# Kernel tuning notes

Measured on AMD Instinct MI355X. Metric: run time of the kernel, lower is better.

The kernel has to match this reference:

```python
import jax, jax.numpy as jnp
import numpy as np

B, T, S, H, E, V = 32, 64, 64, 512, 512, 32000

def setup_inputs() -> dict:
    key = jax.random.key(0)
    ks = jax.random.split(key, 16)
    sd = 0.02
    return {
        "inputs": jax.random.randint(ks[0], (B, T), 0, V),
        "encoder_outputs": jax.random.normal(ks[1], (B, S, 2 * H), jnp.float32),
        "h0": jax.random.normal(ks[2], (B, H), jnp.float32),
        "c0": jax.random.normal(ks[3], (B, H), jnp.float32),
        "emb": jax.random.normal(ks[4], (V, E), jnp.float32) * sd,
        "W_ih": jax.random.normal(ks[5], (4 * H, E), jnp.float32) * sd,
        "W_hh": jax.random.normal(ks[6], (4 * H, H), jnp.float32) * sd,
        "b_ih": jnp.zeros((4 * H,), jnp.float32),
        "b_hh": jnp.zeros((4 * H,), jnp.float32),
        "W_att": jax.random.normal(ks[7], (2 * H, H), jnp.float32) * sd,
        "W_comb": jax.random.normal(ks[8], (H, 3 * H), jnp.float32) * sd,
        "b_comb": jnp.zeros((H,), jnp.float32),
        "W_out": jax.random.normal(ks[9], (V, H), jnp.float32) * sd,
        "b_out": jnp.zeros((V,), jnp.float32),
    }

def reference(inputs, encoder_outputs, h0, c0, emb, W_ih, W_hh, b_ih, b_hh,
              W_att, W_comb, b_comb, W_out, b_out):
    x = emb[inputs]                      # [B,T,E]
    xs = jnp.swapaxes(x, 0, 1)           # [T,B,E] for scan

    def step(carry, x_t):
        h, c = carry
        # torch LSTM gate order: i, f, g, o
        gates = x_t @ W_ih.T + h @ W_hh.T + b_ih + b_hh   # [B,4H]
        i, f, g, o = jnp.split(gates, 4, axis=-1)
        c = jax.nn.sigmoid(f) * c + jax.nn.sigmoid(i) * jnp.tanh(g)
        h = jax.nn.sigmoid(o) * jnp.tanh(c)
        # attention (note: no softmax in original module)
        q = h @ W_att.T                                     # [B,2H]
        w = jnp.einsum('bd,bsd->bs', q, encoder_outputs)    # [B,S]
        applied = jnp.einsum('bs,bsd->bd', w, encoder_outputs)  # [B,2H]
        merged = jnp.concatenate([h, applied], axis=-1)     # [B,3H]
        out = jnp.tanh(merged @ W_comb.T + b_comb)          # [B,H]
        return (h, c), out

    (h, c), outs = jax.lax.scan(step, (h0, c0), xs)
    outs = jnp.swapaxes(outs, 0, 1)      # [B,T,H]
    logits = outs @ W_out.T + b_out      # [B,T,V]
    return logits, h, c
```

## Files before the change

### kernel.cpp

```cpp
#include <hip/hip_runtime.h>
#include <hip/hip_fp16.h>

typedef _Float16 f16;
typedef _Float16 f16x4 __attribute__((ext_vector_type(4)));
typedef _Float16 f16x8 __attribute__((ext_vector_type(8)));
typedef float    f32x4 __attribute__((ext_vector_type(4)));

#define DEV __device__ __forceinline__

constexpr int B = 32, T = 64, S = 64, H = 512, E = 512, V = 32000;
constexpr int BT = B * T;
constexpr int G4 = 4 * H;
constexpr int NBLK = 64;

DEV float sigf(float x) { return 1.f / (1.f + expf(-x)); }

DEV unsigned long long ld_u64_cg(const unsigned long long* p) {
    return __hip_atomic_load(p, __ATOMIC_RELAXED, __HIP_MEMORY_SCOPE_AGENT);
}
DEV unsigned int ld_u32_cg(const unsigned int* p) {
    return __hip_atomic_load(p, __ATOMIC_RELAXED, __HIP_MEMORY_SCOPE_AGENT);
}
DEV void st_u32_cg(unsigned int* p, unsigned int v) {
    __hip_atomic_store(p, v, __ATOMIC_RELAXED, __HIP_MEMORY_SCOPE_AGENT);
}


__global__ __launch_bounds__(256) void cvt_f16(const float* __restrict__ s,
                                               f16* __restrict__ d, int n4) {
    for (int i = blockIdx.x * blockDim.x + threadIdx.x; i < n4;
         i += gridDim.x * blockDim.x) {
        float4 v = ((const float4*)s)[i];
        f16x4 o = {(f16)v.x, (f16)v.y, (f16)v.z, (f16)v.w};
        ((f16x4*)d)[i] = o;
    }
}

__global__ __launch_bounds__(256) void pack_wfrag(const float* __restrict__ W,
                                                  f16* __restrict__ Wf) {
    int id = blockIdx.x * 256 + threadIdx.x;
    if (id >= NBLK * 2 * 16 * 64) return;
    int lane = id & 63;
    int ks = (id >> 6) & 15;
    int ni = (id >> 10) & 1;
    int n = id >> 11;
    int cl = ni * 16 + (lane & 15);
    int ul = cl >> 2, g = cl & 3;
    int unit = n * 8 + ul;
    int k = ks * 32 + (lane >> 4) * 8;
    const float* src = W + (size_t)(g * 512 + unit) * 512 + k;
    float4 a = *(const float4*)src;
    float4 b = *(const float4*)(src + 4);
    f16x8 o = {(f16)a.x, (f16)a.y, (f16)a.z, (f16)a.w,
               (f16)b.x, (f16)b.y, (f16)b.z, (f16)b.w};
    *(f16x8*)(Wf + (size_t)id * 8) = o;
}

__global__ __launch_bounds__(256) void gather_x(const int* __restrict__ tok,
                                                const float* __restrict__ emb,
                                                f16* __restrict__ x) {
    int id = blockIdx.x * blockDim.x + threadIdx.x;
    if (id >= BT * (E / 4)) return;
    int row = id >> 7;
    int e4 = (id & 127) * 4;
    int t = tok[row];
    float4 v = *(const float4*)(emb + (size_t)t * E + e4);
    f16x4 o = {(f16)v.x, (f16)v.y, (f16)v.z, (f16)v.w};
    ((f16x4*)x)[id] = o;
}

__global__ __launch_bounds__(256) void init_h0(const float* __restrict__ h0,
                                               f16* __restrict__ xbuf,
                                               unsigned int* __restrict__ fl) {
    int i = blockIdx.x * 256 + threadIdx.x;
    if (i < B * H) {
        int nn = i >> 8;
        int bb = (i >> 3) & 31;
        int ul = i & 7;
        xbuf[i] = (f16)h0[bb * 512 + nn * 8 + ul];
    }
    if (i < NBLK) fl[i] = 0u;
}


template <bool BIAS, bool B2, bool TANH, bool PERM, bool MSWAP, typename OUT>
__global__ __launch_bounds__(256) void gemm_bt(
    const f16* __restrict__ A, int lda, const f16* __restrict__ W, int ldw,
    OUT* __restrict__ C, int ldc, int K, const float* __restrict__ bias1,
    const float* __restrict__ bias2) {
    __shared__ f16 smA[128 * 32];
    __shared__ f16 smB[128 * 32];
    const int tid = threadIdx.x;
    const int lane = tid & 63;
    const int wv = tid >> 6;
    const int wr = wv >> 1, wc = wv & 1;
    const int m0 = (MSWAP ? blockIdx.x : blockIdx.y) * 128;
    const int n0 = (MSWAP ? blockIdx.y : blockIdx.x) * 128;

    const int ar0 = tid >> 2;
    const int kq = (tid & 3) * 8;

    f32x4 acc[4][4];
#pragma unroll
    for (int m = 0; m < 4; m++)
#pragma unroll
        for (int n = 0; n < 4; n++) acc[m][n] = {0.f, 0.f, 0.f, 0.f};

    const int arow = wr * 64 + (lane & 15);
    const int brow = wc * 64 + (lane & 15);
    const int kk = (lane >> 4) * 8;

    const int ksteps = K >> 5;
    for (int s = 0; s < ksteps; ++s) {
        const int k0 = s * 32;
        const f16* Ag = A + (size_t)(m0 + ar0) * lda + k0 + kq;
        const f16* Wg = W + (size_t)(n0 + ar0) * ldw + k0 + kq;
        uint4 va0 = *(const uint4*)Ag;
        uint4 va1 = *(const uint4*)(Ag + (size_t)64 * lda);
        uint4 vb0 = *(const uint4*)Wg;
        uint4 vb1 = *(const uint4*)(Wg + (size_t)64 * ldw);
        __syncthreads();
        *(uint4*)(smA + tid * 8) = va0;
        *(uint4*)(smA + (tid + 256) * 8) = va1;
        *(uint4*)(smB + tid * 8) = vb0;
        *(uint4*)(smB + (tid + 256) * 8) = vb1;
        __syncthreads();
        f16x8 af[4], bfr[4];
#pragma unroll
        for (int m = 0; m < 4; m++)
            af[m] = *(const f16x8*)(smA + (arow + m * 16) * 32 + kk);
#pragma unroll
        for (int n = 0; n < 4; n++)
            bfr[n] = *(const f16x8*)(smB + (brow + n * 16) * 32 + kk);
#pragma unroll
        for (int m = 0; m < 4; m++)
#pragma unroll
            for (int n = 0; n < 4; n++)
                acc[m][n] = __builtin_amdgcn_mfma_f32_16x16x32_f16(
                    af[m], bfr[n], acc[m][n], 0, 0, 0);
    }

    const int fr = lane & 15, fq = lane >> 4;
#pragma unroll
    for (int m = 0; m < 4; m++) {
        const int row0 = m0 + wr * 64 + m * 16 + fq * 4;
#pragma unroll
        for (int n = 0; n < 4; n++) {
            const int col = n0 + wc * 64 + n * 16 + fr;
            float bb = 0.f;
            if (BIAS) bb += bias1[col];
            if (B2) bb += bias2[col];
            int nb = 0, cl = 0;
            if (PERM) {
                int g = col >> 9;
                int unit = col & 511;
                nb = unit >> 3;
                cl = ((unit & 7) << 2) | g;
            }
#pragma unroll
            for (int r = 0; r < 4; r++) {
                float v = acc[m][n][r] + bb;
                if (TANH) v = tanhf(v);
                if (PERM) {
                    int bt = row0 + r;
                    int b_ = bt >> 6, tt = bt & 63;
                    C[((size_t)(tt * 64 + nb) * 32 + b_) * 32 + cl] = (OUT)v;
                } else {
                    C[(size_t)(row0 + r) * ldc + col] = (OUT)v;
                }
            }
        }
    }
}


__global__ __launch_bounds__(256, 1) void lstm_scan6(
    const float* __restrict__ gxp, const f16* __restrict__ Wfrag,
    const float* __restrict__ c0, f16* __restrict__ xbuf,
    unsigned int* __restrict__ flags, f16* __restrict__ merged,
    float* __restrict__ hout, float* __restrict__ cout) {
    const int n = blockIdx.x;
    const int tid = threadIdx.x;
    const int lane = tid & 63, wv = tid >> 6;
    const int mi = wv >> 1, ni = wv & 1;
    __shared__ f16 hst[32][520];
    __shared__ float gl[32][32];

    f16x8 bf[16];
    const f16* wbase = Wfrag + (size_t)((n * 2 + ni) * 16) * 512 + lane * 8;
#pragma unroll
    for (int ks = 0; ks < 16; ks++) bf[ks] = *(const f16x8*)(wbase + ks * 512);

    const int bb = tid >> 3, ul = tid & 7;
    const int unit = n * 8 + ul;
    float c = c0[bb * 512 + unit];
    float h = 0.f;

    const int sb = (tid & 63) >> 1;
    const int su0 = (tid & 1) * 4;

    const int arow = mi * 16 + (lane & 15);
    const int kcol0 = (lane >> 4) * 8;
    const int fr = lane & 15, fq = lane >> 4;

    for (int t = 0; t < T; ++t) {
        float4 gx4 = *(const float4*)(gxp +
                                      ((size_t)(t * NBLK + n) * 32 + bb) * 32 +
                                      ul * 4);
        for (;;) {
            unsigned int v = ld_u32_cg(flags + lane);
            if (__all(v >= (unsigned int)t)) break;
            __builtin_amdgcn_s_sleep(1);
        }
        asm volatile("" ::: "memory");
        const unsigned long long* src =
            (const unsigned long long*)(xbuf + (t & 1) * (B * H));
        unsigned long long v[16];
#pragma unroll
        for (int i = 0; i < 16; i++) v[i] = ld_u64_cg(src + i * 256 + tid);
#pragma unroll
        for (int i = 0; i < 16; i++) {
            int np = i * 4 + wv;
            *(unsigned long long*)(&hst[sb][np * 8 + su0]) = v[i];
        }
        __syncthreads();
        f32x4 acc0 = {0.f, 0.f, 0.f, 0.f}, acc1 = {0.f, 0.f, 0.f, 0.f};
#pragma unroll
        for (int ks = 0; ks < 16; ks++) {
            f16x8 af = *(const f16x8*)(&hst[arow][ks * 32 + kcol0]);
            if (ks & 1)
                acc1 = __builtin_amdgcn_mfma_f32_16x16x32_f16(af, bf[ks], acc1,
                                                              0, 0, 0);
            else
                acc0 = __builtin_amdgcn_mfma_f32_16x16x32_f16(af, bf[ks], acc0,
                                                              0, 0, 0);
        }
#pragma unroll
        for (int r = 0; r < 4; r++)
            gl[mi * 16 + fq * 4 + r][ni * 16 + fr] = acc0[r] + acc1[r];
        __syncthreads();
        float4 gv = *(const float4*)&gl[bb][ul * 4];
        float gi = gv.x + gx4.x;
        float gf = gv.y + gx4.y;
        float gg = gv.z + gx4.z;
        float go = gv.w + gx4.w;
        c = sigf(gf) * c + sigf(gi) * tanhf(gg);
        h = sigf(go) * tanhf(c);
        f16 hh = (f16)h;
        unsigned hv = (unsigned)__builtin_bit_cast(unsigned short, hh);
        unsigned other = (unsigned)__shfl_xor((int)hv, 1);
        f16* xn = xbuf + ((t + 1) & 1) * (B * H);
        if ((ul & 1) == 0) {
            st_u32_cg((unsigned int*)(xn + n * 256 + bb * 8 + ul),
                      hv | (other << 16));
        }
        if (t < T - 1) {
            asm volatile("s_waitcnt vmcnt(0)" ::: "memory");
            __syncthreads();
            if (tid == 0) st_u32_cg(flags + n, (unsigned int)(t + 1));
        } else {
            __syncthreads();
        }
        merged[(size_t)(bb * 64 + t) * 1536 + unit] = hh;
    }
    hout[bb * 512 + unit] = h;
    cout[bb * 512 + unit] = c;
}


__global__ __launch_bounds__(256) void attn_apply(const float* __restrict__ q,
                                                  const float* __restrict__ enc,
                                                  f16* __restrict__ merged) {
    const int bt = blockIdx.x;
    const int b = bt >> 6;
    const int tid = threadIdx.x;
    __shared__ float qs[1024];
    __shared__ float ws[64];

    const float* qrow = q + (size_t)bt * 1024;
    *(float4*)(qs + tid * 4) = *(const float4*)(qrow + tid * 4);
    __syncthreads();

    const int wv = tid >> 6, lane = tid & 63;
    const float* encb = enc + (size_t)b * S * 1024;
    for (int s = wv * 16; s < wv * 16 + 16; ++s) {
        const float* er = encb + (size_t)s * 1024;
        float p = 0.f;
#pragma unroll
        for (int i = 0; i < 16; ++i) p += qs[lane + 64 * i] * er[lane + 64 * i];
#pragma unroll
        for (int off = 32; off; off >>= 1) p += __shfl_xor(p, off);
        if (lane == 0) ws[s] = p;
    }
    __syncthreads();

    float a0 = 0.f, a1 = 0.f, a2 = 0.f, a3 = 0.f;
    for (int s = 0; s < 64; ++s) {
        float w = ws[s];
        const float* er = encb + (size_t)s * 1024;
        a0 += w * er[tid];
        a1 += w * er[tid + 256];
        a2 += w * er[tid + 512];
        a3 += w * er[tid + 768];
    }
    f16* mrow = merged + (size_t)bt * 1536 + 512;
    mrow[tid] = (f16)a0;
    mrow[tid + 256] = (f16)a1;
    mrow[tid + 512] = (f16)a2;
    mrow[tid + 768] = (f16)a3;
}


extern "C" void kernel_launch(void* const* d_in, const int* in_sizes, int n_in,
                              void* d_out, int out_size, void* d_ws,
                              size_t ws_size, hipStream_t stream) {
    const int* tok = (const int*)d_in[0];
    const float* enc = (const float*)d_in[1];
    const float* h0 = (const float*)d_in[2];
    const float* c0 = (const float*)d_in[3];
    const float* emb = (const float*)d_in[4];
    const float* W_ih = (const float*)d_in[5];
    const float* W_hh = (const float*)d_in[6];
    const float* b_ih = (const float*)d_in[7];
    const float* b_hh = (const float*)d_in[8];
    const float* W_att = (const float*)d_in[9];
    const float* W_comb = (const float*)d_in[10];
    const float* b_comb = (const float*)d_in[11];
    const float* W_out = (const float*)d_in[12];
    const float* b_out = (const float*)d_in[13];

    float* out_logits = (float*)d_out;
    float* out_h = out_logits + (size_t)BT * V;
    float* out_c = out_h + (size_t)B * H;

    char* p = (char*)d_ws;
    auto alloc = [&](size_t bytes) -> void* {
        void* r = (void*)p;
        p += (bytes + 255) & ~(size_t)255;
        return r;
    };
    f16* W_ih_h = (f16*)alloc((size_t)G4 * E * 2);
    f16* Wfrag = (f16*)alloc((size_t)NBLK * 2 * 16 * 64 * 8 * 2);
    f16* W_att_h = (f16*)alloc((size_t)1024 * 512 * 2);
    f16* W_comb_h = (f16*)alloc((size_t)512 * 1536 * 2);
    f16* W_out_h = (f16*)alloc((size_t)V * 512 * 2);
    f16* x_h = (f16*)alloc((size_t)BT * E * 2);
    float* gxp = (float*)alloc((size_t)T * NBLK * 32 * 32 * 4);
    f16* merged = (f16*)alloc((size_t)BT * 1536 * 2);
    float* qbuf = (float*)alloc((size_t)BT * 1024 * 4);
    f16* outs_h = (f16*)alloc((size_t)BT * 512 * 2);
    f16* xbuf = (f16*)alloc((size_t)2 * B * H * 2);
    unsigned int* flags = (unsigned int*)alloc(256);

    cvt_f16<<<512, 256, 0, stream>>>(W_ih, W_ih_h, G4 * E / 4);
    cvt_f16<<<512, 256, 0, stream>>>(W_att, W_att_h, 1024 * 512 / 4);
    cvt_f16<<<512, 256, 0, stream>>>(W_comb, W_comb_h, 512 * 1536 / 4);
    cvt_f16<<<2048, 256, 0, stream>>>(W_out, W_out_h, V * 512 / 4);
    pack_wfrag<<<512, 256, 0, stream>>>(W_hh, Wfrag);
    gather_x<<<1024, 256, 0, stream>>>(tok, emb, x_h);
    init_h0<<<64, 256, 0, stream>>>(h0, xbuf, flags);

    gemm_bt<true, true, false, true, false, float>
        <<<dim3(16, 16), 256, 0, stream>>>(x_h, E, W_ih_h, E, gxp, 0, E, b_ih,
                                           b_hh);

    lstm_scan6<<<NBLK, 256, 0, stream>>>(gxp, Wfrag, c0, xbuf, flags, merged,
                                         out_h, out_c);

    gemm_bt<false, false, false, false, false, float>
        <<<dim3(8, 16), 256, 0, stream>>>(merged, 1536, W_att_h, 512, qbuf,
                                          1024, 512, nullptr, nullptr);

    attn_apply<<<BT, 256, 0, stream>>>(qbuf, enc, merged);

    gemm_bt<true, false, true, false, false, f16>
        <<<dim3(4, 16), 256, 0, stream>>>(merged, 1536, W_comb_h, 1536, outs_h,
                                          512, 1536, b_comb, nullptr);

    gemm_bt<true, false, false, false, true, float>
        <<<dim3(16, 250), 256, 0, stream>>>(outs_h, 512, W_out_h, 512,
                                            out_logits, V, 512, b_out,
                                            nullptr);
}
```

Baseline: 557.3 us.

## Read h directly in MFMA layout, stage scan outputs, fuse W_out conversion into GEMM

Result: slower. 608.8 us (+9.2%).

```diff
diff --git a/kernel.cpp b/kernel.cpp
--- a/kernel.cpp
+++ b/kernel.cpp
@@ -82,12 +82,24 @@
     if (i < NBLK) fl[i] = 0u;
 }
 
-
-template <bool BIAS, bool B2, bool TANH, bool PERM, bool MSWAP, typename OUT>
+__global__ __launch_bounds__(256) void scatter_h(const f16* __restrict__ mtmp,
+                                                 f16* __restrict__ merged) {
+    int c = blockIdx.x * 256 + threadIdx.x;
+    if (c >= T * NBLK * B) return;
+    int bb = c & 31;
+    int n = (c >> 5) & 63;
+    int t = c >> 11;
+    uint4 v = ((const uint4*)mtmp)[c];
+    ((uint4*)merged)[(size_t)(bb * 64 + t) * 192 + n] = v;
+}
+
+
+template <bool BIAS, bool B2, bool TANH, bool PERM, bool MSWAP, bool WF32,
+          typename OUT>
 __global__ __launch_bounds__(256) void gemm_bt(
-    const f16* __restrict__ A, int lda, const f16* __restrict__ W, int ldw,
-    OUT* __restrict__ C, int ldc, int K, const float* __restrict__ bias1,
-    const float* __restrict__ bias2) {
+    const f16* __restrict__ A, int lda, const f16* __restrict__ W,
+    const float* __restrict__ W32, int ldw, OUT* __restrict__ C, int ldc,
+    int K, const float* __restrict__ bias1, const float* __restrict__ bias2) {
     __shared__ f16 smA[128 * 32];
     __shared__ f16 smB[128 * 32];
     const int tid = threadIdx.x;
@@ -114,11 +126,26 @@
     for (int s = 0; s < ksteps; ++s) {
         const int k0 = s * 32;
         const f16* Ag = A + (size_t)(m0 + ar0) * lda + k0 + kq;
-        const f16* Wg = W + (size_t)(n0 + ar0) * ldw + k0 + kq;
         uint4 va0 = *(const uint4*)Ag;
         uint4 va1 = *(const uint4*)(Ag + (size_t)64 * lda);
-        uint4 vb0 = *(const uint4*)Wg;
-        uint4 vb1 = *(const uint4*)(Wg + (size_t)64 * ldw);
+        uint4 vb0, vb1;
+        if (WF32) {
+            const float* Wg = W32 + (size_t)(n0 + ar0) * ldw + k0 + kq;
+            float4 b00 = *(const float4*)Wg;
+            float4 b01 = *(const float4*)(Wg + 4);
+            float4 b10 = *(const float4*)(Wg + (size_t)64 * ldw);
+            float4 b11 = *(const float4*)(Wg + (size_t)64 * ldw + 4);
+            f16x8 h0v = {(f16)b00.x, (f16)b00.y, (f16)b00.z, (f16)b00.w,
+                         (f16)b01.x, (f16)b01.y, (f16)b01.z, (f16)b01.w};
+            f16x8 h1v = {(f16)b10.x, (f16)b10.y, (f16)b10.z, (f16)b10.w,
+                         (f16)b11.x, (f16)b11.y, (f16)b11.z, (f16)b11.w};
+            vb0 = __builtin_bit_cast(uint4, h0v);
+            vb1 = __builtin_bit_cast(uint4, h1v);
+        } else {
+            const f16* Wg = W + (size_t)(n0 + ar0) * ldw + k0 + kq;
+            vb0 = *(const uint4*)Wg;
+            vb1 = *(const uint4*)(Wg + (size_t)64 * ldw);
+        }
         __syncthreads();
         *(uint4*)(smA + tid * 8) = va0;
         *(uint4*)(smA + (tid + 256) * 8) = va1;
@@ -174,16 +201,15 @@
 }
 
 
-__global__ __launch_bounds__(256, 1) void lstm_scan6(
+__global__ __launch_bounds__(256, 1) void lstm_scan7(
     const float* __restrict__ gxp, const f16* __restrict__ Wfrag,
     const float* __restrict__ c0, f16* __restrict__ xbuf,
-    unsigned int* __restrict__ flags, f16* __restrict__ merged,
+    unsigned int* __restrict__ flags, f16* __restrict__ mtmp,
     float* __restrict__ hout, float* __restrict__ cout) {
     const int n = blockIdx.x;
     const int tid = threadIdx.x;
     const int lane = tid & 63, wv = tid >> 6;
     const int mi = wv >> 1, ni = wv & 1;
-    __shared__ f16 hst[32][520];
     __shared__ float gl[32][32];
 
     f16x8 bf[16];
@@ -196,12 +222,9 @@
     float c = c0[bb * 512 + unit];
     float h = 0.f;
 
-    const int sb = (tid & 63) >> 1;
-    const int su0 = (tid & 1) * 4;
-
-    const int arow = mi * 16 + (lane & 15);
-    const int kcol0 = (lane >> 4) * 8;
     const int fr = lane & 15, fq = lane >> 4;
+    const int arow = mi * 16 + fr;
+    const int ubase = fq * 64 + arow * 2;
 
     for (int t = 0; t < T; ++t) {
         float4 gx4 = *(const float4*)(gxp +
@@ -213,21 +236,20 @@
             __builtin_amdgcn_s_sleep(1);
         }
         asm volatile("" ::: "memory");
-        const unsigned long long* src =
+        const unsigned long long* xb =
             (const unsigned long long*)(xbuf + (t & 1) * (B * H));
-        unsigned long long v[16];
-#pragma unroll
-        for (int i = 0; i < 16; i++) v[i] = ld_u64_cg(src + i * 256 + tid);
-#pragma unroll
-        for (int i = 0; i < 16; i++) {
-            int np = i * 4 + wv;
-            *(unsigned long long*)(&hst[sb][np * 8 + su0]) = v[i];
-        }
-        __syncthreads();
+        unsigned long long lo[16], hi[16];
+#pragma unroll
+        for (int ks = 0; ks < 16; ks++) {
+            lo[ks] = ld_u64_cg(xb + ks * 256 + ubase);
+            hi[ks] = ld_u64_cg(xb + ks * 256 + ubase + 1);
+        }
         f32x4 acc0 = {0.f, 0.f, 0.f, 0.f}, acc1 = {0.f, 0.f, 0.f, 0.f};
 #pragma unroll
         for (int ks = 0; ks < 16; ks++) {
-            f16x8 af = *(const f16x8*)(&hst[arow][ks * 32 + kcol0]);
+            f16x4 l4 = __builtin_bit_cast(f16x4, lo[ks]);
+            f16x4 h4 = __builtin_bit_cast(f16x4, hi[ks]);
+            f16x8 af = {l4.x, l4.y, l4.z, l4.w, h4.x, h4.y, h4.z, h4.w};
             if (ks & 1)
                 acc1 = __builtin_amdgcn_mfma_f32_16x16x32_f16(af, bf[ks], acc1,
                                                               0, 0, 0);
@@ -258,10 +280,8 @@
             asm volatile("s_waitcnt vmcnt(0)" ::: "memory");
             __syncthreads();
             if (tid == 0) st_u32_cg(flags + n, (unsigned int)(t + 1));
-        } else {
-            __syncthreads();
-        }
-        merged[(size_t)(bb * 64 + t) * 1536 + unit] = hh;
+        }
+        mtmp[(size_t)(t * NBLK + n) * 256 + tid] = hh;
     }
     hout[bb * 512 + unit] = h;
     cout[bb * 512 + unit] = c;
@@ -343,42 +363,44 @@
     f16* Wfrag = (f16*)alloc((size_t)NBLK * 2 * 16 * 64 * 8 * 2);
     f16* W_att_h = (f16*)alloc((size_t)1024 * 512 * 2);
     f16* W_comb_h = (f16*)alloc((size_t)512 * 1536 * 2);
-    f16* W_out_h = (f16*)alloc((size_t)V * 512 * 2);
     f16* x_h = (f16*)alloc((size_t)BT * E * 2);
     float* gxp = (float*)alloc((size_t)T * NBLK * 32 * 32 * 4);
     f16* merged = (f16*)alloc((size_t)BT * 1536 * 2);
     float* qbuf = (float*)alloc((size_t)BT * 1024 * 4);
     f16* outs_h = (f16*)alloc((size_t)BT * 512 * 2);
     f16* xbuf = (f16*)alloc((size_t)2 * B * H * 2);
+    f16* mtmp = (f16*)alloc((size_t)T * NBLK * 256 * 2);
     unsigned int* flags = (unsigned int*)alloc(256);
 
     cvt_f16<<<512, 256, 0, stream>>>(W_ih, W_ih_h, G4 * E / 4);
     cvt_f16<<<512, 256, 0, stream>>>(W_att, W_att_h, 1024 * 512 / 4);
     cvt_f16<<<512, 256, 0, stream>>>(W_comb, W_comb_h, 512 * 1536 / 4);
-    cvt_f16<<<2048, 256, 0, stream>>>(W_out, W_out_h, V * 512 / 4);
     pack_wfrag<<<512, 256, 0, stream>>>(W_hh, Wfrag);
     gather_x<<<1024, 256, 0, stream>>>(tok, emb, x_h);
     init_h0<<<64, 256, 0, stream>>>(h0, xbuf, flags);
 
-    gemm_bt<true, true, false, true, false, float>
-        <<<dim3(16, 16), 256, 0, stream>>>(x_h, E, W_ih_h, E, gxp, 0, E, b_ih,
-                                           b_hh);
-
-    lstm_scan6<<<NBLK, 256, 0, stream>>>(gxp, Wfrag, c0, xbuf, flags, merged,
+    gemm_bt<true, true, false, true, false, false, float>
+        <<<dim3(16, 16), 256, 0, stream>>>(x_h, E, W_ih_h, nullptr, E, gxp, 0,
+                                           E, b_ih, b_hh);
+
+    lstm_scan7<<<NBLK, 256, 0, stream>>>(gxp, Wfrag, c0, xbuf, flags, mtmp,
                                          out_h, out_c);
 
-    gemm_bt<false, false, false, false, false, float>
-        <<<dim3(8, 16), 256, 0, stream>>>(merged, 1536, W_att_h, 512, qbuf,
-                                          1024, 512, nullptr, nullptr);
+    scatter_h<<<1024, 256, 0, stream>>>(mtmp, merged);
+
+    gemm_bt<false, false, false, false, false, false, float>
+        <<<dim3(8, 16), 256, 0, stream>>>(merged, 1536, W_att_h, nullptr, 512,
+                                          qbuf, 1024, 512, nullptr, nullptr);
 
     attn_apply<<<BT, 256, 0, stream>>>(qbuf, enc, merged);
 
-    gemm_bt<true, false, true, false, false, f16>
-        <<<dim3(4, 16), 256, 0, stream>>>(merged, 1536, W_comb_h, 1536, outs_h,
-                                          512, 1536, b_comb, nullptr);
-
-    gemm_bt<true, false, false, false, true, float>
-        <<<dim3(16, 250), 256, 0, stream>>>(outs_h, 512, W_out_h, 512,
+    gemm_bt<true, false, true, false, false, false, f16>
+        <<<dim3(4, 16), 256, 0, stream>>>(merged, 1536, W_comb_h, nullptr,
+                                          1536, outs_h, 512, 1536, b_comb,
+                                          nullptr);
+
+    gemm_bt<true, false, false, false, true, true, float>
+        <<<dim3(16, 250), 256, 0, stream>>>(outs_h, 512, nullptr, W_out, 512,
                                             out_logits, V, 512, b_out,
                                             nullptr);
 }
```

## Run LSTM recurrence on 16 blocks of 1024 threads with LDS-resident weights

Applied to the files above, without the earlier changes.

After: 870.7 us (median of 2 runs). 56.2% more time.

```diff
diff --git a/kernel.cpp b/kernel.cpp
--- a/kernel.cpp
+++ b/kernel.cpp
@@ -11,7 +11,7 @@
 constexpr int B = 32, T = 64, S = 64, H = 512, E = 512, V = 32000;
 constexpr int BT = B * T;
 constexpr int G4 = 4 * H;
-constexpr int NBLK = 64;
+constexpr int NB2 = 16;
 
 DEV float sigf(float x) { return 1.f / (1.f + expf(-x)); }
 
@@ -39,14 +39,12 @@
 __global__ __launch_bounds__(256) void pack_wfrag(const float* __restrict__ W,
                                                   f16* __restrict__ Wf) {
     int id = blockIdx.x * 256 + threadIdx.x;
-    if (id >= NBLK * 2 * 16 * 64) return;
+    if (id >= 128 * 16 * 64) return;
     int lane = id & 63;
     int ks = (id >> 6) & 15;
-    int ni = (id >> 10) & 1;
-    int n = id >> 11;
-    int cl = ni * 16 + (lane & 15);
-    int ul = cl >> 2, g = cl & 3;
-    int unit = n * 8 + ul;
+    int nt = id >> 10;
+    int colg = nt * 16 + (lane & 15);
+    int unit = colg >> 2, g = colg & 3;
     int k = ks * 32 + (lane >> 4) * 8;
     const float* src = W + (size_t)(g * 512 + unit) * 512 + k;
     float4 a = *(const float4*)src;
@@ -74,12 +72,12 @@
                                                unsigned int* __restrict__ fl) {
     int i = blockIdx.x * 256 + threadIdx.x;
     if (i < B * H) {
-        int nn = i >> 8;
-        int bb = (i >> 3) & 31;
-        int ul = i & 7;
-        xbuf[i] = (f16)h0[bb * 512 + nn * 8 + ul];
-    }
-    if (i < NBLK) fl[i] = 0u;
+        int nn = i >> 10;
+        int bb = (i >> 5) & 31;
+        int ul = i & 31;
+        xbuf[i] = (f16)h0[bb * 512 + nn * 32 + ul];
+    }
+    if (i < NB2) fl[i] = 0u;
 }
 
 
@@ -174,7 +172,7 @@
 }
 
 
-__global__ __launch_bounds__(256, 1) void lstm_scan6(
+__global__ __launch_bounds__(1024, 1) void lstm_scan8(
     const float* __restrict__ gxp, const f16* __restrict__ Wfrag,
     const float* __restrict__ c0, f16* __restrict__ xbuf,
     unsigned int* __restrict__ flags, f16* __restrict__ merged,
@@ -182,57 +180,60 @@
     const int n = blockIdx.x;
     const int tid = threadIdx.x;
     const int lane = tid & 63, wv = tid >> 6;
-    const int mi = wv >> 1, ni = wv & 1;
-    __shared__ f16 hst[32][520];
-    __shared__ float gl[32][32];
-
-    f16x8 bf[16];
-    const f16* wbase = Wfrag + (size_t)((n * 2 + ni) * 16) * 512 + lane * 8;
-#pragma unroll
-    for (int ks = 0; ks < 16; ks++) bf[ks] = *(const f16x8*)(wbase + ks * 512);
-
-    const int bb = tid >> 3, ul = tid & 7;
-    const int unit = n * 8 + ul;
+    const int mi = wv >> 3, ni = wv & 7;
+    __shared__ f16 wlds[65536];
+    __shared__ float gl[32][128];
+
+    {
+        const f16* wsrc = Wfrag + (size_t)n * 65536;
+#pragma unroll
+        for (int i = 0; i < 8; i++)
+            *(f16x8*)(wlds + (size_t)(i * 1024 + tid) * 8) =
+                *(const f16x8*)(wsrc + (size_t)(i * 1024 + tid) * 8);
+    }
+
+    const int bb = tid >> 5, ul = tid & 31;
+    const int unit = n * 32 + ul;
     float c = c0[bb * 512 + unit];
     float h = 0.f;
 
-    const int sb = (tid & 63) >> 1;
-    const int su0 = (tid & 1) * 4;
-
-    const int arow = mi * 16 + (lane & 15);
-    const int kcol0 = (lane >> 4) * 8;
     const int fr = lane & 15, fq = lane >> 4;
+    const int arow = mi * 16 + fr;
+    const int ubase = arow * 8 + fq * 2;
+    const f16* wbase = wlds + (size_t)(ni * 16) * 512 + lane * 8;
+
+    __syncthreads();
 
     for (int t = 0; t < T; ++t) {
-        float4 gx4 = *(const float4*)(gxp +
-                                      ((size_t)(t * NBLK + n) * 32 + bb) * 32 +
-                                      ul * 4);
+        float4 gx4 = *(const float4*)(
+            gxp + ((size_t)(t * 64 + n * 4 + (ul >> 3)) * 32 + bb) * 32 +
+            (ul & 7) * 4);
         for (;;) {
-            unsigned int v = ld_u32_cg(flags + lane);
+            unsigned int v = ld_u32_cg(flags + (lane & 15));
             if (__all(v >= (unsigned int)t)) break;
             __builtin_amdgcn_s_sleep(1);
         }
         asm volatile("" ::: "memory");
-        const unsigned long long* src =
+        const unsigned long long* xb =
             (const unsigned long long*)(xbuf + (t & 1) * (B * H));
-        unsigned long long v[16];
-#pragma unroll
-        for (int i = 0; i < 16; i++) v[i] = ld_u64_cg(src + i * 256 + tid);
-#pragma unroll
-        for (int i = 0; i < 16; i++) {
-            int np = i * 4 + wv;
-            *(unsigned long long*)(&hst[sb][np * 8 + su0]) = v[i];
-        }
-        __syncthreads();
+        unsigned long long alo[16], ahi[16];
+#pragma unroll
+        for (int ks = 0; ks < 16; ks++) {
+            alo[ks] = ld_u64_cg(xb + ks * 256 + ubase);
+            ahi[ks] = ld_u64_cg(xb + ks * 256 + ubase + 1);
+        }
         f32x4 acc0 = {0.f, 0.f, 0.f, 0.f}, acc1 = {0.f, 0.f, 0.f, 0.f};
 #pragma unroll
         for (int ks = 0; ks < 16; ks++) {
-            f16x8 af = *(const f16x8*)(&hst[arow][ks * 32 + kcol0]);
+            f16x4 l4 = __builtin_bit_cast(f16x4, alo[ks]);
+            f16x4 h4 = __builtin_bit_cast(f16x4, ahi[ks]);
+            f16x8 af = {l4.x, l4.y, l4.z, l4.w, h4.x, h4.y, h4.z, h4.w};
+            f16x8 bfr = *(const f16x8*)(wbase + ks * 512);
             if (ks & 1)
-                acc1 = __builtin_amdgcn_mfma_f32_16x16x32_f16(af, bf[ks], acc1,
+                acc1 = __builtin_amdgcn_mfma_f32_16x16x32_f16(af, bfr, acc1,
                                                               0, 0, 0);
             else
-                acc0 = __builtin_amdgcn_mfma_f32_16x16x32_f16(af, bf[ks], acc0,
+                acc0 = __builtin_amdgcn_mfma_f32_16x16x32_f16(af, bfr, acc0,
                                                               0, 0, 0);
         }
 #pragma unroll
@@ -250,10 +251,9 @@
         unsigned hv = (unsigned)__builtin_bit_cast(unsigned short, hh);
         unsigned other = (unsigned)__shfl_xor((int)hv, 1);
         f16* xn = xbuf + ((t + 1) & 1) * (B * H);
-        if ((ul & 1) == 0) {
-            st_u32_cg((unsigned int*)(xn + n * 256 + bb * 8 + ul),
+        if ((ul & 1) == 0)
+            st_u32_cg((unsigned int*)(xn + n * 1024 + bb * 32 + ul),
                       hv | (other << 16));
-        }
         if (t < T - 1) {
             asm volatile("s_waitcnt vmcnt(0)" ::: "memory");
             __syncthreads();
@@ -340,12 +340,12 @@
         return r;
     };
     f16* W_ih_h = (f16*)alloc((size_t)G4 * E * 2);
-    f16* Wfrag = (f16*)alloc((size_t)NBLK * 2 * 16 * 64 * 8 * 2);
+    f16* Wfrag = (f16*)alloc((size_t)128 * 16 * 64 * 8 * 2);
     f16* W_att_h = (f16*)alloc((size_t)1024 * 512 * 2);
     f16* W_comb_h = (f16*)alloc((size_t)512 * 1536 * 2);
     f16* W_out_h = (f16*)alloc((size_t)V * 512 * 2);
     f16* x_h = (f16*)alloc((size_t)BT * E * 2);
-    float* gxp = (float*)alloc((size_t)T * NBLK * 32 * 32 * 4);
+    float* gxp = (float*)alloc((size_t)T * 64 * 32 * 32 * 4);
     f16* merged = (f16*)alloc((size_t)BT * 1536 * 2);
     float* qbuf = (float*)alloc((size_t)BT * 1024 * 4);
     f16* outs_h = (f16*)alloc((size_t)BT * 512 * 2);
@@ -364,7 +364,7 @@
         <<<dim3(16, 16), 256, 0, stream>>>(x_h, E, W_ih_h, E, gxp, 0, E, b_ih,
                                            b_hh);
 
-    lstm_scan6<<<NBLK, 256, 0, stream>>>(gxp, Wfrag, c0, xbuf, flags, merged,
+    lstm_scan8<<<NB2, 1024, 0, stream>>>(gxp, Wfrag, c0, xbuf, flags, merged,
                                          out_h, out_c);
 
     gemm_bt<false, false, false, false, false, float>
```
